# Kernel tuning notes

Measured on AMD Instinct MI355X. Metric: run time of the kernel, lower is better.

## Reference

```python
import math
import jax, jax.numpy as jnp
import numpy as np

N_HEAD = 16

def setup_inputs() -> dict:
    key = jax.random.key(0)
    ks = jax.random.split(key, 3)
    B, T, C = 2, 2048, 1024
    x = jax.random.normal(ks[0], (B, T, C), dtype=jnp.float32)
    W_kqv = jax.random.normal(ks[1], (3 * C, C), dtype=jnp.float32) * 0.02
    b_kqv = jnp.zeros((3 * C,), dtype=jnp.float32)
    W_proj = jax.random.normal(ks[2], (C, C), dtype=jnp.float32) * 0.02
    b_proj = jnp.zeros((C,), dtype=jnp.float32)
    return {"x": x, "W_kqv": W_kqv, "b_kqv": b_kqv, "W_proj": W_proj, "b_proj": b_proj}

def reference(x, W_kqv, b_kqv, W_proj, b_proj):
    B, T, C = x.shape
    nh = N_HEAD
    hd = C // nh
    # fused QKV projection, then view [B,T,nh,3*hd] and slice into k,q,v
    kqv = (x @ W_kqv.T + b_kqv).reshape(B, T, nh, 3, hd)
    k = kqv[..., 0, :]  # [B,T,nh,hd]
    q = kqv[..., 1, :]
    v = kqv[..., 2, :]
    scale = 1.0 / math.sqrt(hd)
    att = jnp.einsum("bthd,bshd->bhts", q, k) * scale  # [B,nh,T,T]
    causal = jnp.tril(jnp.ones((T, T), dtype=bool))
    att = jnp.where(causal[None, None], att, -jnp.inf)
    att = jax.nn.softmax(att, axis=-1)
    y = jnp.einsum("bhts,bshd->bthd", att, v).reshape(B, T, C)
    return y @ W_proj.T + b_proj
```

## Files before the change

kernel.cpp:

```cpp
#include <hip/hip_runtime.h>

#define TSEQ 2048
#define NHEAD 16
#define HD 64
#define CDIM 1024
#define BT 4096

typedef unsigned short u16;
typedef __bf16 bf16x8 __attribute__((ext_vector_type(8)));
typedef float f32x4 __attribute__((ext_vector_type(4)));
typedef float f32x16 __attribute__((ext_vector_type(16)));

union Frag {
  int4 i4;
  bf16x8 b;
  u16 u[8];
};

__device__ __forceinline__ u16 f2b(float f) {
  union { float f; unsigned u; } x;
  x.f = f;
  unsigned r = x.u + 0x7fffu + ((x.u >> 16) & 1u);
  return (u16)(r >> 16);
}

#define N4X 1048576
#define N4W1 786432
#define N4W2 262144
__global__ void cvt3_kernel(const float* __restrict__ x, const float* __restrict__ w1,
                            const float* __restrict__ w2, u16* __restrict__ ox,
                            u16* __restrict__ o1, u16* __restrict__ o2) {
  int i = blockIdx.x * blockDim.x + threadIdx.x;
  int stride = gridDim.x * blockDim.x;
  for (int idx = i; idx < N4X + N4W1 + N4W2; idx += stride) {
    const float4* src;
    ushort4* dst;
    int k;
    if (idx < N4X) { src = (const float4*)x; dst = (ushort4*)ox; k = idx; }
    else if (idx < N4X + N4W1) { src = (const float4*)w1; dst = (ushort4*)o1; k = idx - N4X; }
    else { src = (const float4*)w2; dst = (ushort4*)o2; k = idx - N4X - N4W1; }
    float4 f = src[k];
    ushort4 o;
    o.x = f2b(f.x); o.y = f2b(f.y); o.z = f2b(f.z); o.w = f2b(f.w);
    dst[k] = o;
  }
}

__device__ __forceinline__ void gload_lds16(const u16* g, u16* l) {
  __builtin_amdgcn_global_load_lds((__attribute__((address_space(1))) void*)g,
                                   (__attribute__((address_space(3))) void*)l, 16, 0, 0);
}

__device__ __forceinline__ void gemm_tiles(const u16* __restrict__ A, const u16* __restrict__ Bw,
                                           int K, int m0, int n0, u16* Ash, u16* Bsh,
                                           f32x4 acc[4][4]) {
  const int tid = threadIdx.x;
  const int lane = tid & 63;
  const int w = tid >> 6;
  const int wr = (w >> 1) * 64, wc = (w & 1) * 64;
  const int lr = lane & 15;
  const int lkb = (lane >> 4) << 3;
  const int r0 = tid >> 2;
  const int c0 = (tid & 3) << 3;

  for (int k0 = 0; k0 < K; k0 += 32) {
#pragma unroll
    for (int s = 0; s < 2; s++) {
      gload_lds16(&A[(size_t)(m0 + s * 64 + r0) * K + k0 + c0], &Ash[(s * 256 + tid) * 8]);
      gload_lds16(&Bw[(size_t)(n0 + s * 64 + r0) * K + k0 + c0], &Bsh[(s * 256 + tid) * 8]);
    }
    __syncthreads();
    Frag af[4], bfr[4];
#pragma unroll
    for (int i = 0; i < 4; i++) {
      af[i].i4 = *(const int4*)&Ash[(wr + i * 16 + lr) * 32 + lkb];
      bfr[i].i4 = *(const int4*)&Bsh[(wc + i * 16 + lr) * 32 + lkb];
    }
#pragma unroll
    for (int mf = 0; mf < 4; mf++)
#pragma unroll
      for (int nf = 0; nf < 4; nf++)
        acc[mf][nf] = __builtin_amdgcn_mfma_f32_16x16x32_bf16(af[mf].b, bfr[nf].b, acc[mf][nf], 0, 0, 0);
    __syncthreads();
  }
}

__global__ __launch_bounds__(256) void gemm_kqv(const u16* __restrict__ xb, const u16* __restrict__ wb,
                                                const float* __restrict__ bias,
                                                u16* __restrict__ qb, u16* __restrict__ kb,
                                                u16* __restrict__ vtb) {
  __shared__ u16 Ash[128 * 32];
  __shared__ u16 Bsh[128 * 32];
  const int m0 = blockIdx.y * 128, n0 = blockIdx.x * 128;
  f32x4 acc[4][4];
#pragma unroll
  for (int i = 0; i < 4; i++)
#pragma unroll
    for (int j = 0; j < 4; j++) acc[i][j] = (f32x4){0.f, 0.f, 0.f, 0.f};

  gemm_tiles(xb, wb, CDIM, m0, n0, Ash, Bsh, acc);

  const int tid = threadIdx.x;
  const int lane = tid & 63;
  const int w = tid >> 6;
  const int wr = (w >> 1) * 64, wc = (w & 1) * 64;
  const int lr = lane & 15;
  const int rbase = (lane >> 4) << 2;
#pragma unroll
  for (int mf = 0; mf < 4; mf++) {
#pragma unroll
    for (int nf = 0; nf < 4; nf++) {
      f32x4 a = acc[mf][nf];
      int n = n0 + wc + nf * 16 + lr;
      float bval = bias[n];
      int h = n / 192;
      int rem = n - h * 192;
      int s = rem >> 6;
      int d = rem & 63;
      float scale = (s == 1) ? 0.125f : 1.f;
      u16* dst = (s == 0) ? kb : qb;
#pragma unroll
      for (int r = 0; r < 4; r++) {
        int m = m0 + wr + mf * 16 + rbase + r;
        int bb = m >> 11, tt = m & 2047;
        int bh = (bb << 4) + h;
        u16 val = f2b((a[r] + bval) * scale);
        if (s == 2) {
          int t63 = tt & 63;
          int c = (t63 & 51) | ((t63 & 8) >> 1) | ((t63 & 4) << 1);
          vtb[((size_t)bh * HD + d) * TSEQ + (tt & ~63) + c] = val;
        } else {
          dst[((size_t)bh * TSEQ + tt) * HD + d] = val;
        }
      }
    }
  }
}

__global__ __launch_bounds__(256) void gemm_proj(const u16* __restrict__ yb, const u16* __restrict__ wb,
                                                 const float* __restrict__ bias,
                                                 float* __restrict__ out) {
  __shared__ u16 Ash[128 * 32];
  __shared__ u16 Bsh[128 * 32];
  const int m0 = blockIdx.y * 128, n0 = blockIdx.x * 128;
  f32x4 acc[4][4];
#pragma unroll
  for (int i = 0; i < 4; i++)
#pragma unroll
    for (int j = 0; j < 4; j++) acc[i][j] = (f32x4){0.f, 0.f, 0.f, 0.f};

  gemm_tiles(yb, wb, CDIM, m0, n0, Ash, Bsh, acc);

  const int tid = threadIdx.x;
  const int lane = tid & 63;
  const int w = tid >> 6;
  const int wr = (w >> 1) * 64, wc = (w & 1) * 64;
  const int lr = lane & 15;
  const int rbase = (lane >> 4) << 2;
#pragma unroll
  for (int mf = 0; mf < 4; mf++) {
#pragma unroll
    for (int nf = 0; nf < 4; nf++) {
      f32x4 a = acc[mf][nf];
      int n = n0 + wc + nf * 16 + lr;
      float bval = bias[n];
#pragma unroll
      for (int r = 0; r < 4; r++) {
        int m = m0 + wr + mf * 16 + rbase + r;
        out[(size_t)m * CDIM + n] = a[r] + bval;
      }
    }
  }
}

__global__ __launch_bounds__(256, 2) void attn_kernel(const u16* __restrict__ qb,
                                                      const u16* __restrict__ kb,
                                                      const u16* __restrict__ vtb,
                                                      u16* __restrict__ yb) {
  __shared__ u16 Ksh[2][64 * 64];
  __shared__ u16 Vsh[2][64 * 64];

  const int tid = threadIdx.x;
  const int lane = tid & 63;
  const int w = tid >> 6;
  const int l31 = lane & 31;
  const int hi32 = lane >> 5;
  const int swz = l31 & 7;

  const int jj = blockIdx.x;
  const int bh = jj & 31;
  const int cls = jj >> 5;
  const int qbk = (cls < 8) ? (15 - cls) : (cls - 8);
  const int q0w = qbk * 128 + w * 32;
  const int LN = 2 * qbk + 2;
  const int jd = q0w >> 6;
  const int qg = q0w + l31;

  const u16* Qp = qb + (size_t)bh * TSEQ * HD;
  const u16* Kp = kb + (size_t)bh * TSEQ * HD;
  const u16* Vt = vtb + (size_t)bh * HD * TSEQ;

  Frag qf[4];
#pragma unroll
  for (int k = 0; k < 4; k++)
    qf[k].i4 = *(const int4*)&Qp[(size_t)(q0w + l31) * HD + k * 16 + hi32 * 8];

  f32x16 O0, O1;
  float lp = 0.f;
#pragma unroll
  for (int i = 0; i < 16; i++) { O0[i] = 0.f; O1[i] = 0.f; }

#define STAGE(B, JT)                                                                 \
  {                                                                                  \
    const int kvb = (JT) * 64;                                                       \
    _Pragma("unroll") for (int p = 0; p < 2; p++) {                                  \
      int c = tid + p * 256;                                                         \
      int row = c >> 3, c16 = c & 7;                                                 \
      int gofs = (c16 ^ (row & 7)) << 3;                                             \
      gload_lds16(&Kp[(size_t)(kvb + row) * HD + gofs], &Ksh[B][c * 8]);             \
      gload_lds16(&Vt[(size_t)row * TSEQ + kvb + gofs], &Vsh[B][c * 8]);             \
    }                                                                                \
  }

#define PACK2(dst, SV, base)                                                         \
    asm("v_cvt_pk_bf16_f32 %0, %1, %2" : "=v"(dst.i4.x) : "v"(SV[base + 0]), "v"(SV[base + 1])); \
    asm("v_cvt_pk_bf16_f32 %0, %1, %2" : "=v"(dst.i4.y) : "v"(SV[base + 2]), "v"(SV[base + 3])); \
    asm("v_cvt_pk_bf16_f32 %0, %1, %2" : "=v"(dst.i4.z) : "v"(SV[base + 4]), "v"(SV[base + 5])); \
    asm("v_cvt_pk_bf16_f32 %0, %1, %2" : "=v"(dst.i4.w) : "v"(SV[base + 6]), "v"(SV[base + 7]));

  STAGE(0, 0)
  int cur = 0;
  for (int jt = 0; jt < LN; ++jt) {
    __syncthreads();
    const int kv0 = jt * 64;
    const bool act = (jt <= jd);
    const bool run1 = (kv0 + 32) <= (q0w + 31);

    Frag ka0[4], ka1[4], vf0[4], vf1[4];
    if (act) {
      const u16* Kt = Ksh[cur];
      const u16* Vl = Vsh[cur];
#pragma unroll
      for (int k = 0; k < 4; k++) {
        int ch = ((2 * k + hi32) ^ swz) << 3;
        ka0[k].i4 = *(const int4*)&Kt[l31 * 64 + ch];
        vf0[k].i4 = *(const int4*)&Vl[l31 * 64 + ch];
        vf1[k].i4 = *(const int4*)&Vl[(32 + l31) * 64 + ch];
      }
      if (run1) {
#pragma unroll
        for (int k = 0; k < 4; k++) {
          int ch = ((2 * k + hi32) ^ swz) << 3;
          ka1[k].i4 = *(const int4*)&Kt[(32 + l31) * 64 + ch];
        }
      }
    }
    __builtin_amdgcn_sched_barrier(0);
    if (jt + 1 < LN) STAGE(cur ^ 1, jt + 1)
    __builtin_amdgcn_sched_barrier(0);
    if (act) {
      const bool diag = (jt == jd);
      f32x16 S;
#pragma unroll
      for (int i = 0; i < 16; i++) S[i] = 0.f;
      __builtin_amdgcn_s_setprio(1);
#pragma unroll
      for (int k = 0; k < 4; k++)
        S = __builtin_amdgcn_mfma_f32_32x32x16_bf16(ka0[k].b, qf[k].b, S, 0, 0, 0);
      __builtin_amdgcn_s_setprio(0);
      if (diag) {
#pragma unroll
        for (int reg = 0; reg < 16; reg++) {
          int crow = (reg & 3) + 8 * (reg >> 2) + 4 * hi32;
          S[reg] = (kv0 + crow <= qg) ? __expf(S[reg]) : 0.f;
        }
      } else {
#pragma unroll
        for (int reg = 0; reg < 16; reg++) S[reg] = __expf(S[reg]);
      }
#pragma unroll
      for (int reg = 0; reg < 16; reg++) lp += S[reg];
      Frag pa[2];
      PACK2(pa[0], S, 0)
      PACK2(pa[1], S, 8)
      __builtin_amdgcn_s_setprio(1);
#pragma unroll
      for (int k = 0; k < 2; k++) {
        O0 = __builtin_amdgcn_mfma_f32_32x32x16_bf16(pa[k].b, vf0[k].b, O0, 0, 0, 0);
        O1 = __builtin_amdgcn_mfma_f32_32x32x16_bf16(pa[k].b, vf1[k].b, O1, 0, 0, 0);
      }
      __builtin_amdgcn_s_setprio(0);
      if (run1) {
        f32x16 T;
#pragma unroll
        for (int i = 0; i < 16; i++) T[i] = 0.f;
        __builtin_amdgcn_s_setprio(1);
#pragma unroll
        for (int k = 0; k < 4; k++)
          T = __builtin_amdgcn_mfma_f32_32x32x16_bf16(ka1[k].b, qf[k].b, T, 0, 0, 0);
        __builtin_amdgcn_s_setprio(0);
        if (diag) {
#pragma unroll
          for (int reg = 0; reg < 16; reg++) {
            int crow = (reg & 3) + 8 * (reg >> 2) + 4 * hi32;
            T[reg] = (kv0 + 32 + crow <= qg) ? __expf(T[reg]) : 0.f;
          }
        } else {
#pragma unroll
          for (int reg = 0; reg < 16; reg++) T[reg] = __expf(T[reg]);
        }
#pragma unroll
        for (int reg = 0; reg < 16; reg++) lp += T[reg];
        Frag pb[2];
        PACK2(pb[0], T, 0)
        PACK2(pb[1], T, 8)
        __builtin_amdgcn_s_setprio(1);
#pragma unroll
        for (int k = 0; k < 2; k++) {
          O0 = __builtin_amdgcn_mfma_f32_32x32x16_bf16(pb[k].b, vf0[k + 2].b, O0, 0, 0, 0);
          O1 = __builtin_amdgcn_mfma_f32_32x32x16_bf16(pb[k].b, vf1[k + 2].b, O1, 0, 0, 0);
        }
        __builtin_amdgcn_s_setprio(0);
      }
    }
    cur ^= 1;
  }
#undef STAGE
#undef PACK2

  float lpt = lp + __shfl_xor(lp, 32);
  const int b = bh >> 4, h = bh & 15;
#pragma unroll
  for (int reg = 0; reg < 16; reg++) {
    int qlocal = (reg & 3) + 8 * (reg >> 2) + 4 * hi32;
    float invr = 1.f / __shfl(lpt, qlocal);
    int t = q0w + qlocal;
    size_t rowoff = ((size_t)(b * TSEQ + t) << 10) + (h << 6);
    yb[rowoff + l31] = f2b(O0[reg] * invr);
    yb[rowoff + 32 + l31] = f2b(O1[reg] * invr);
  }
}

extern "C" void kernel_launch(void* const* d_in, const int* in_sizes, int n_in,
                              void* d_out, int out_size, void* d_ws, size_t ws_size,
                              hipStream_t stream) {
  const float* x = (const float*)d_in[0];
  const float* Wkqv = (const float*)d_in[1];
  const float* bkqv = (const float*)d_in[2];
  const float* Wproj = (const float*)d_in[3];
  const float* bproj = (const float*)d_in[4];
  float* out = (float*)d_out;

  u16* ws = (u16*)d_ws;
  u16* xb = ws;
  u16* wkqvb = xb + 4194304;
  u16* wprojb = wkqvb + 3145728;
  u16* qb = wprojb + 1048576;
  u16* kb = qb + 4194304;
  u16* vtb = kb + 4194304;
  u16* yb = vtb + 4194304;

  cvt3_kernel<<<2048, 256, 0, stream>>>(x, Wkqv, Wproj, xb, wkqvb, wprojb);
  gemm_kqv<<<dim3(24, 32), 256, 0, stream>>>(xb, wkqvb, bkqv, qb, kb, vtb);
  attn_kernel<<<512, 256, 0, stream>>>(qb, kb, vtb, yb);
  gemm_proj<<<dim3(8, 32), 256, 0, stream>>>(yb, wprojb, bproj, out);
}
```

Measured before the change: 108.9 us.

## Double-buffer GEMM LDS tiles with swizzled layout and vectorize V-transpose stores

The shared GEMM tile loop now uses two LDS buffers. The next K-slice is prefetched with global_load_lds while MFMAs run on the current slice, and there is a single barrier per iteration instead of two. The LDS chunk layout is XOR-swizzled on both the async writes and the fragment reads to reduce bank conflicts. The KQV epilogue also packs the four consecutive V-transpose values into one ushort4 store. This doubles the GEMM LDS footprint, which may reduce occupancy, and it depends on the compiler waiting for the async LDS loads before the barrier.

Measured after the change: 98.07 us. 1.11x faster.

```diff
diff --git a/kernel.cpp b/kernel.cpp
--- a/kernel.cpp
+++ b/kernel.cpp
@@ -52,45 +52,55 @@
 }
 
 __device__ __forceinline__ void gemm_tiles(const u16* __restrict__ A, const u16* __restrict__ Bw,
-                                           int K, int m0, int n0, u16* Ash, u16* Bsh,
+                                           int K, int m0, int n0,
+                                           u16 (*__restrict__ Ash)[128 * 32],
+                                           u16 (*__restrict__ Bsh)[128 * 32],
                                            f32x4 acc[4][4]) {
   const int tid = threadIdx.x;
   const int lane = tid & 63;
   const int w = tid >> 6;
   const int wr = (w >> 1) * 64, wc = (w & 1) * 64;
   const int lr = lane & 15;
-  const int lkb = (lane >> 4) << 3;
+  const int hi = lane >> 4;
   const int r0 = tid >> 2;
-  const int c0 = (tid & 3) << 3;
-
+  const int cS = ((tid & 3) ^ ((tid >> 3) & 3)) << 3;
+  const int frg = (hi ^ ((lr >> 1) & 3)) << 3;
+
+#define GSTAGE(B, KO)                                                                 \
+  { _Pragma("unroll") for (int s = 0; s < 2; s++) {                                   \
+      gload_lds16(&A[(size_t)(m0 + s * 64 + r0) * K + (KO) + cS], &Ash[B][(s * 256 + tid) * 8]); \
+      gload_lds16(&Bw[(size_t)(n0 + s * 64 + r0) * K + (KO) + cS], &Bsh[B][(s * 256 + tid) * 8]); \
+  } }
+
+  GSTAGE(0, 0)
+  int cur = 0;
   for (int k0 = 0; k0 < K; k0 += 32) {
-#pragma unroll
-    for (int s = 0; s < 2; s++) {
-      gload_lds16(&A[(size_t)(m0 + s * 64 + r0) * K + k0 + c0], &Ash[(s * 256 + tid) * 8]);
-      gload_lds16(&Bw[(size_t)(n0 + s * 64 + r0) * K + k0 + c0], &Bsh[(s * 256 + tid) * 8]);
-    }
     __syncthreads();
     Frag af[4], bfr[4];
 #pragma unroll
     for (int i = 0; i < 4; i++) {
-      af[i].i4 = *(const int4*)&Ash[(wr + i * 16 + lr) * 32 + lkb];
-      bfr[i].i4 = *(const int4*)&Bsh[(wc + i * 16 + lr) * 32 + lkb];
-    }
+      af[i].i4 = *(const int4*)&Ash[cur][(wr + i * 16 + lr) * 32 + frg];
+      bfr[i].i4 = *(const int4*)&Bsh[cur][(wc + i * 16 + lr) * 32 + frg];
+    }
+    __builtin_amdgcn_sched_barrier(0);
+    if (k0 + 32 < K) GSTAGE(cur ^ 1, k0 + 32)
+    __builtin_amdgcn_sched_barrier(0);
 #pragma unroll
     for (int mf = 0; mf < 4; mf++)
 #pragma unroll
       for (int nf = 0; nf < 4; nf++)
         acc[mf][nf] = __builtin_amdgcn_mfma_f32_16x16x32_bf16(af[mf].b, bfr[nf].b, acc[mf][nf], 0, 0, 0);
-    __syncthreads();
-  }
+    cur ^= 1;
+  }
+#undef GSTAGE
 }
 
 __global__ __launch_bounds__(256) void gemm_kqv(const u16* __restrict__ xb, const u16* __restrict__ wb,
                                                 const float* __restrict__ bias,
                                                 u16* __restrict__ qb, u16* __restrict__ kb,
                                                 u16* __restrict__ vtb) {
-  __shared__ u16 Ash[128 * 32];
-  __shared__ u16 Bsh[128 * 32];
+  __shared__ u16 Ash[2][128 * 32];
+  __shared__ u16 Bsh[2][128 * 32];
   const int m0 = blockIdx.y * 128, n0 = blockIdx.x * 128;
   f32x4 acc[4][4];
 #pragma unroll
@@ -117,21 +127,22 @@
       int rem = n - h * 192;
       int s = rem >> 6;
       int d = rem & 63;
-      float scale = (s == 1) ? 0.125f : 1.f;
-      u16* dst = (s == 0) ? kb : qb;
-#pragma unroll
-      for (int r = 0; r < 4; r++) {
-        int m = m0 + wr + mf * 16 + rbase + r;
-        int bb = m >> 11, tt = m & 2047;
-        int bh = (bb << 4) + h;
-        u16 val = f2b((a[r] + bval) * scale);
-        if (s == 2) {
-          int t63 = tt & 63;
-          int c = (t63 & 51) | ((t63 & 8) >> 1) | ((t63 & 4) << 1);
-          vtb[((size_t)bh * HD + d) * TSEQ + (tt & ~63) + c] = val;
-        } else {
-          dst[((size_t)bh * TSEQ + tt) * HD + d] = val;
-        }
+      int m00 = m0 + wr + mf * 16 + rbase;
+      int bb = m00 >> 11, tt = m00 & 2047;
+      int bh = (bb << 4) + h;
+      if (s == 2) {
+        int t63 = tt & 63;
+        int c = (t63 & 51) | ((t63 & 8) >> 1) | ((t63 & 4) << 1);
+        ushort4 v4;
+        v4.x = f2b(a[0] + bval); v4.y = f2b(a[1] + bval);
+        v4.z = f2b(a[2] + bval); v4.w = f2b(a[3] + bval);
+        *(ushort4*)&vtb[((size_t)bh * HD + d) * TSEQ + (tt & ~63) + c] = v4;
+      } else {
+        float scale = (s == 1) ? 0.125f : 1.f;
+        u16* dst = (s == 0) ? kb : qb;
+#pragma unroll
+        for (int r = 0; r < 4; r++)
+          dst[((size_t)bh * TSEQ + tt + r) * HD + d] = f2b((a[r] + bval) * scale);
       }
     }
   }
@@ -140,8 +151,8 @@
 __global__ __launch_bounds__(256) void gemm_proj(const u16* __restrict__ yb, const u16* __restrict__ wb,
                                                  const float* __restrict__ bias,
                                                  float* __restrict__ out) {
-  __shared__ u16 Ash[128 * 32];
-  __shared__ u16 Bsh[128 * 32];
+  __shared__ u16 Ash[2][128 * 32];
+  __shared__ u16 Bsh[2][128 * 32];
   const int m0 = blockIdx.y * 128, n0 = blockIdx.x * 128;
   f32x4 acc[4][4];
 #pragma unroll
```
